# Optimization experiments

Hardware: AMD Instinct MI355X
Metric: run time of the kernel (lower is better)

The kernel has to match this reference:

```python
import jax, jax.numpy as jnp
import numpy as np

B, T, D = 8, 2048, 128


def setup_inputs() -> dict:
    key = jax.random.key(0)
    kq, kk, kv = jax.random.split(key, 3)
    q = jax.random.normal(kq, (B, T, D), dtype=jnp.float32)
    k = jax.random.normal(kk, (B, T, D), dtype=jnp.float32)
    v = jax.random.normal(kv, (B, T, D), dtype=jnp.float32)
    # causal mask, broadcast over batch; 0 -> masked
    mask = jnp.tril(jnp.ones((T, T), dtype=jnp.int32))[None, :, :]
    mode = jnp.float32(0.5)  # learnable scalar parameter (init 0.5)
    return {"q": q, "k": k, "v": v, "mask": mask, "mode": mode}


def reference(q, k, v, mask, mode):
    scale = D ** (-0.5)
    # meson score: -(Q K^T) * scale
    meson = -jnp.einsum("btd,bsd->bts", q, k) * scale
    # baryon score: Q against K with feature dim rolled by 1
    k_perm = jnp.roll(k, shift=1, axis=-1)
    baryon = jnp.einsum("btd,bsd->bts", q, k_perm) * scale
    alpha = jax.nn.sigmoid(mode)
    attn = alpha * meson + (1.0 - alpha) * baryon
    attn = jnp.where(mask == 0, -jnp.inf, attn)
    attn = jax.nn.softmax(attn, axis=-1)
    return jnp.einsum("bts,bsd->btd", attn, v)
```

## Files before the change

kernel.cpp:

```cpp
#include <hip/hip_runtime.h>
#include <hip/hip_bf16.h>
#include <cstdint>
#include <cstddef>


typedef __attribute__((ext_vector_type(8))) short short8;
typedef __attribute__((ext_vector_type(4))) float f32x4;

#define T_DIM 2048
#define D_DIM 128
#define B_DIM 8
#define SEGT 8
#define POSLOTS_PER_B 112
#define MLSLOTS_PER_B 144
#define LOG2E 1.4426950408889634f

__device__ __forceinline__ unsigned short f2bf(float f) {
  unsigned u = __builtin_bit_cast(unsigned, f);
  u += 0x7FFFu + ((u >> 16) & 1u);
  return (unsigned short)(u >> 16);
}
__device__ __forceinline__ float bf2f(unsigned short u) {
  return __uint_as_float(((unsigned)u) << 16);
}
__device__ __forceinline__ void gload_lds16(const void* g, void* l) {
  __builtin_amdgcn_global_load_lds(
      (const __attribute__((address_space(1))) unsigned int*)g,
      (__attribute__((address_space(3))) unsigned int*)l, 16, 0, 0);
}

__global__ __launch_bounds__(256) void prep_all(
    const float* __restrict__ q, const float* __restrict__ k, const float* __restrict__ v,
    const float* __restrict__ modep,
    unsigned short* __restrict__ qbf, unsigned short* __restrict__ kbf,
    unsigned short* __restrict__ vt)
{
  __shared__ unsigned short tile[64 * 136];
  const int b = blockIdx.x, s0 = blockIdx.y * 64;
  const int tid = threadIdx.x;
  const float alpha = 1.f / (1.f + __expf(-modep[0]));
  const float scale = 0.08838834764831845f;
  const float ca = -alpha * scale * LOG2E, cb = (1.f - alpha) * scale * LOG2E;

#pragma unroll
  for (int u = 0; u < 4; ++u) {
    int c = u * 256 + tid;
    int r = c >> 4, c8 = c & 15;
    size_t row = (size_t)b * T_DIM + s0 + r;
    float4 ka = *(const float4*)(k + row * D_DIM + c8 * 8);
    float4 kb2 = *(const float4*)(k + row * D_DIM + c8 * 8 + 4);
    short8 ko = { (short)f2bf(ka.x), (short)f2bf(ka.y), (short)f2bf(ka.z), (short)f2bf(ka.w),
                  (short)f2bf(kb2.x), (short)f2bf(kb2.y), (short)f2bf(kb2.z), (short)f2bf(kb2.w) };
    *(short8*)(kbf + row * D_DIM + c8 * 8) = ko;
    const float* qr = q + row * D_DIM;
    float e[9];
    float4 f0 = *(const float4*)(qr + c8 * 8);
    float4 f1 = *(const float4*)(qr + c8 * 8 + 4);
    e[0] = f0.x; e[1] = f0.y; e[2] = f0.z; e[3] = f0.w;
    e[4] = f1.x; e[5] = f1.y; e[6] = f1.z; e[7] = f1.w;
    e[8] = qr[(c8 * 8 + 8) & 127];
    short8 qo;
#pragma unroll
    for (int j = 0; j < 8; ++j) qo[j] = (short)f2bf(ca * e[j] + cb * e[j + 1]);
    *(short8*)(qbf + row * D_DIM + c8 * 8) = qo;
    float4 va = *(const float4*)(v + row * D_DIM + c8 * 8);
    float4 vb2 = *(const float4*)(v + row * D_DIM + c8 * 8 + 4);
    short8 vo = { (short)f2bf(va.x), (short)f2bf(va.y), (short)f2bf(va.z), (short)f2bf(va.w),
                  (short)f2bf(vb2.x), (short)f2bf(vb2.y), (short)f2bf(vb2.z), (short)f2bf(vb2.w) };
    *(short8*)(tile + r * 136 + c8 * 8) = vo;
  }
  __syncthreads();
#pragma unroll
  for (int u = 0; u < 8; ++u) {
    int c = u * 256 + tid;
    int d = c >> 4, sq = c & 15;
    ushort4 o = { tile[(sq * 4 + 0) * 136 + d], tile[(sq * 4 + 1) * 136 + d],
                  tile[(sq * 4 + 2) * 136 + d], tile[(sq * 4 + 3) * 136 + d] };
    *(ushort4*)(vt + ((size_t)b * D_DIM + d) * T_DIM + s0 + sq * 4) = o;
  }
}

__global__ __launch_bounds__(128, 2) void attn_kernel(
    const unsigned short* __restrict__ qbf, const unsigned short* __restrict__ kbf,
    const unsigned short* __restrict__ vt, float* __restrict__ out,
    unsigned short* __restrict__ po, float* __restrict__ ml)
{
  __shared__ uint4 smem4[2304];
  char* smem = (char*)smem4;
  const int tid = threadIdx.x;
  const int w = tid >> 6, lane = tid & 63;
  const int t16 = lane & 15, g = lane >> 4;
  const int b = blockIdx.x;
  const int c = 31 - (int)blockIdx.y;
  const int s = blockIdx.z;
  const int nt = 2 * c + 2;
  const int nseg = (c + 4) >> 2;
  if (s >= nseg) return;
  const int t0 = s * SEGT;
  const int t1 = min(nt, t0 + SEGT);
  const int qbw = c * 64 + w * 32;

  char* pw = smem + 32768 + w * 2048;
  const unsigned short* kbase = kbf + (size_t)b * T_DIM * D_DIM;
  const unsigned short* vbase = vt + (size_t)b * D_DIM * T_DIM;

  short8 qf[2][4];
#pragma unroll
  for (int mt = 0; mt < 2; ++mt) {
    const unsigned short* qr = qbf + ((size_t)b * T_DIM + qbw + mt * 16 + t16) * D_DIM + g * 8;
#pragma unroll
    for (int dd = 0; dd < 4; ++dd) qf[mt][dd] = *(const short8*)(qr + dd * 32);
  }

  f32x4 acc[2][8];
#pragma unroll
  for (int mt = 0; mt < 2; ++mt)
#pragma unroll
    for (int dt = 0; dt < 8; ++dt) acc[mt][dt] = (f32x4){0.f, 0.f, 0.f, 0.f};
  float mrun[2][4], lsum[2][4];
#pragma unroll
  for (int mt = 0; mt < 2; ++mt)
#pragma unroll
    for (int r = 0; r < 4; ++r) { mrun[mt][r] = -1e30f; lsum[mt][r] = 0.f; }

  auto stage = [&](int cur, int kt) {
    const int kv0 = kt * 32;
    char* kb = smem + cur * 8192;
    char* vb = smem + 16384 + cur * 8192;
#pragma unroll
    for (int u = 0; u < 4; ++u) {
      int s_loc = w * 16 + u * 4 + (lane >> 4);
      int slot = (lane & 15) ^ (s_loc & 7);
      gload_lds16(kbase + (size_t)(kv0 + s_loc) * D_DIM + slot * 8,
                  kb + w * 4096 + u * 1024);
    }
#pragma unroll
    for (int u = 0; u < 4; ++u) {
      int d_loc = w * 64 + u * 16 + (lane >> 2);
      int vslot = (lane & 3) ^ (d_loc & 3);
      gload_lds16(vbase + (size_t)d_loc * T_DIM + kv0 + vslot * 8,
                  vb + w * 4096 + u * 1024);
    }
  };

  stage(0, t0);
  __syncthreads();
  int cur = 0;

  for (int kt = t0; kt < t1; ++kt) {
    if (kt + 1 < t1) stage(cur ^ 1, kt + 1);
    const int kv0 = kt * 32;

    if (kv0 <= qbw + 31) {
      char* kb = smem + cur * 8192;
      char* vb = smem + 16384 + cur * 8192;

      f32x4 sj[2][2];
#pragma unroll
      for (int jt = 0; jt < 2; ++jt) {
        int srow = jt * 16 + t16;
        int rb = srow * 256, swz = (srow & 7) << 4;
        f32x4 s0 = (f32x4){0.f, 0.f, 0.f, 0.f};
        f32x4 s1 = (f32x4){0.f, 0.f, 0.f, 0.f};
#pragma unroll
        for (int dd = 0; dd < 4; ++dd) {
          short8 kf = *(const short8*)(kb + ((rb + dd * 64 + g * 16) ^ swz));
          s0 = __builtin_amdgcn_mfma_f32_16x16x32_bf16(qf[0][dd], kf, s0, 0, 0, 0);
          s1 = __builtin_amdgcn_mfma_f32_16x16x32_bf16(qf[1][dd], kf, s1, 0, 0, 0);
        }
        sj[0][jt] = s0; sj[1][jt] = s1;
      }

      if (kv0 == qbw) {
#pragma unroll
        for (int mt = 0; mt < 2; ++mt)
#pragma unroll
          for (int jt = 0; jt < 2; ++jt) {
            int sg = kv0 + jt * 16 + t16;
#pragma unroll
            for (int r = 0; r < 4; ++r) {
              int tg = qbw + mt * 16 + 4 * g + r;
              if (sg > tg) sj[mt][jt][r] = -1e30f;
            }
          }
      }

      float lm[2][4];
      int ok = 1;
#pragma unroll
      for (int mt = 0; mt < 2; ++mt)
#pragma unroll
        for (int r = 0; r < 4; ++r) {
          lm[mt][r] = fmaxf(sj[mt][0][r], sj[mt][1][r]);
          ok &= (lm[mt][r] <= mrun[mt][r] + 11.0f);
        }
      if (!__all(ok)) {
#pragma unroll
        for (int mt = 0; mt < 2; ++mt)
#pragma unroll
          for (int r = 0; r < 4; ++r) {
            float tm = lm[mt][r];
            tm = fmaxf(tm, __shfl_xor(tm, 1));
            tm = fmaxf(tm, __shfl_xor(tm, 2));
            tm = fmaxf(tm, __shfl_xor(tm, 4));
            tm = fmaxf(tm, __shfl_xor(tm, 8));
            float mnew = fmaxf(mrun[mt][r], tm);
            float corr = exp2f(mrun[mt][r] - mnew);
            mrun[mt][r] = mnew;
            lsum[mt][r] *= corr;
#pragma unroll
            for (int dt = 0; dt < 8; ++dt) acc[mt][dt][r] *= corr;
          }
      }

#pragma unroll
      for (int mt = 0; mt < 2; ++mt)
#pragma unroll
        for (int jt = 0; jt < 2; ++jt)
#pragma unroll
          for (int r = 0; r < 4; ++r) {
            float p = exp2f(sj[mt][jt][r] - mrun[mt][r]);
            lsum[mt][r] += p;
            int row = 4 * g + r;
            *(unsigned short*)(pw + mt * 1024 + row * 64 +
                               ((jt * 32 + t16 * 2) ^ ((row >> 2) << 4))) = f2bf(p);
          }

      short8 pf0 = *(const short8*)(pw + t16 * 64 + ((g * 16) ^ ((t16 >> 2) << 4)));
      short8 pf1 = *(const short8*)(pw + 1024 + t16 * 64 + ((g * 16) ^ ((t16 >> 2) << 4)));
#pragma unroll
      for (int dt = 0; dt < 8; ++dt) {
        int d = dt * 16 + t16;
        short8 vf = *(const short8*)(vb + d * 64 + ((g * 16) ^ ((d & 3) << 4)));
        acc[0][dt] = __builtin_amdgcn_mfma_f32_16x16x32_bf16(pf0, vf, acc[0][dt], 0, 0, 0);
        acc[1][dt] = __builtin_amdgcn_mfma_f32_16x16x32_bf16(pf1, vf, acc[1][dt], 0, 0, 0);
      }
    }

    __syncthreads();
    cur ^= 1;
  }

  float lred[2][4];
#pragma unroll
  for (int mt = 0; mt < 2; ++mt)
#pragma unroll
    for (int r = 0; r < 4; ++r) {
      float v0 = lsum[mt][r];
      v0 += __shfl_xor(v0, 1);
      v0 += __shfl_xor(v0, 2);
      v0 += __shfl_xor(v0, 4);
      v0 += __shfl_xor(v0, 8);
      lred[mt][r] = v0;
    }

  if (nseg == 1) {
#pragma unroll
    for (int mt = 0; mt < 2; ++mt)
#pragma unroll
      for (int r = 0; r < 4; ++r) {
        float inv = 1.0f / lred[mt][r];
#pragma unroll
        for (int dt = 0; dt < 8; ++dt)
          out[((size_t)b * T_DIM + qbw + mt * 16 + 4 * g + r) * D_DIM + dt * 16 + t16] =
              acc[mt][dt][r] * inv;
      }
  } else {
    int pofs = 0;
    for (int cc = 0; cc < c; ++cc) pofs += ((cc + 4) >> 2) - 1;
    if (s == 0) {
#pragma unroll
      for (int mt = 0; mt < 2; ++mt)
#pragma unroll
        for (int r = 0; r < 4; ++r)
#pragma unroll
          for (int dt = 0; dt < 8; ++dt)
            out[((size_t)b * T_DIM + qbw + mt * 16 + 4 * g + r) * D_DIM + dt * 16 + t16] =
                acc[mt][dt][r];
    } else {
      unsigned short* pob = po + ((size_t)b * POSLOTS_PER_B + pofs + (s - 1)) * 8192;
#pragma unroll
      for (int mt = 0; mt < 2; ++mt)
#pragma unroll
        for (int r = 0; r < 4; ++r) {
          int rb = w * 32 + mt * 16 + 4 * g + r;
#pragma unroll
          for (int dt = 0; dt < 8; ++dt)
            pob[rb * 128 + dt * 16 + t16] = f2bf(acc[mt][dt][r]);
        }
    }
    if (t16 == 0) {
      const size_t mlslot = (size_t)b * MLSLOTS_PER_B + pofs + c + s;
#pragma unroll
      for (int mt = 0; mt < 2; ++mt)
#pragma unroll
        for (int r = 0; r < 4; ++r) {
          int rb = w * 32 + mt * 16 + 4 * g + r;
          ml[mlslot * 128 + rb] = mrun[mt][r];
          ml[mlslot * 128 + 64 + rb] = lred[mt][r];
        }
    }
  }
}

__global__ __launch_bounds__(256) void combine_kernel(
    const unsigned short* __restrict__ po, const float* __restrict__ ml,
    float* __restrict__ out)
{
  const int tid = threadIdx.x;
  const int b = blockIdx.x;
  const int c = 4 + (int)blockIdx.y;
  const int nseg = (c + 4) >> 2;
  int pofs = 0;
  for (int cc = 0; cc < c; ++cc) pofs += ((cc + 4) >> 2) - 1;
  const size_t mlbase = (size_t)b * MLSLOTS_PER_B + pofs + c;
  const size_t pobase = (size_t)b * POSLOTS_PER_B + pofs;

  __shared__ float wgt[64][8];
  if (tid < 64) {
    float M = -1e30f;
    for (int s = 0; s < nseg; ++s)
      M = fmaxf(M, ml[(mlbase + s) * 128 + tid]);
    float L = 0.f;
    for (int s = 0; s < nseg; ++s) {
      float e = exp2f(ml[(mlbase + s) * 128 + tid] - M);
      wgt[tid][s] = e;
      L += e * ml[(mlbase + s) * 128 + 64 + tid];
    }
    float invL = 1.f / L;
    for (int s = 0; s < nseg; ++s) wgt[tid][s] *= invL;
  }
  __syncthreads();

#pragma unroll
  for (int it = 0; it < 4; ++it) {
    int vid = it * 256 + tid;
    int r = vid >> 4, ch = vid & 15;
    float* op = out + ((size_t)b * T_DIM + c * 64 + r) * D_DIM + ch * 8;
    float4 a0 = *(const float4*)op;
    float4 a1 = *(const float4*)(op + 4);
    float w0 = wgt[r][0];
    float o[8] = { w0 * a0.x, w0 * a0.y, w0 * a0.z, w0 * a0.w,
                   w0 * a1.x, w0 * a1.y, w0 * a1.z, w0 * a1.w };
    for (int s = 1; s < nseg; ++s) {
      short8 pv = *(const short8*)(po + (pobase + s - 1) * 8192 + r * 128 + ch * 8);
      float ws = wgt[r][s];
#pragma unroll
      for (int j = 0; j < 8; ++j) o[j] += ws * bf2f((unsigned short)pv[j]);
    }
    *(float4*)op = (float4){o[0], o[1], o[2], o[3]};
    *(float4*)(op + 4) = (float4){o[4], o[5], o[6], o[7]};
  }
}

extern "C" void kernel_launch(void* const* d_in, const int* in_sizes, int n_in,
                              void* d_out, int out_size, void* d_ws, size_t ws_size,
                              hipStream_t stream) {
  const float* q = (const float*)d_in[0];
  const float* k = (const float*)d_in[1];
  const float* v = (const float*)d_in[2];
  const float* mode = (const float*)d_in[4];
  float* out = (float*)d_out;

  char* ws = (char*)d_ws;
  unsigned short* qbf = (unsigned short*)(ws);
  unsigned short* kbf = (unsigned short*)(ws + 4194304);
  unsigned short* vtb = (unsigned short*)(ws + 8388608);
  unsigned short* po  = (unsigned short*)(ws + 12582912);
  float*          ml  = (float*)(ws + 27262976);

  prep_all<<<dim3(B_DIM, T_DIM / 64), 256, 0, stream>>>(q, k, v, mode, qbf, kbf, vtb);
  attn_kernel<<<dim3(B_DIM, 32, SEGT), 128, 0, stream>>>(qbf, kbf, vtb, out, po, ml);
  combine_kernel<<<dim3(B_DIM, 28), 256, 0, stream>>>(po, ml, out);
}
```

Baseline: 56.85 us.

## Switch attention to 32x32x16 MFMA with transposed S and register-shuffled P

Rewrites the attention inner loop to use 32x32x16 bf16 MFMAs that compute S transposed (K as A operand), so each lane owns one query row. The softmax row max and sum then need only a single cross-half shuffle, and P is repacked into the B-operand layout with lane shuffles instead of a round trip through LDS. This removes the per-wave P scratch buffer and the LDS swizzle writes and reads, and widens the K swizzle to 16 slots. Output stores become vectorized per row. The cost is larger accumulator fragments per lane and possible register pressure under the 2-block launch bound.

```diff
diff --git a/kernel.cpp b/kernel.cpp
--- a/kernel.cpp
+++ b/kernel.cpp
@@ -6,6 +6,8 @@
 
 typedef __attribute__((ext_vector_type(8))) short short8;
 typedef __attribute__((ext_vector_type(4))) float f32x4;
+typedef __attribute__((ext_vector_type(16))) float f32x16;
+typedef __attribute__((ext_vector_type(4))) unsigned uint4v;
 
 #define T_DIM 2048
 #define D_DIM 128
@@ -22,6 +24,9 @@
 }
 __device__ __forceinline__ float bf2f(unsigned short u) {
   return __uint_as_float(((unsigned)u) << 16);
+}
+__device__ __forceinline__ unsigned pack2bf(float a, float b) {
+  return (unsigned)f2bf(a) | ((unsigned)f2bf(b) << 16);
 }
 __device__ __forceinline__ void gload_lds16(const void* g, void* l) {
   __builtin_amdgcn_global_load_lds(
@@ -85,11 +90,11 @@
     const unsigned short* __restrict__ vt, float* __restrict__ out,
     unsigned short* __restrict__ po, float* __restrict__ ml)
 {
-  __shared__ uint4 smem4[2304];
+  __shared__ uint4 smem4[2048];
   char* smem = (char*)smem4;
   const int tid = threadIdx.x;
   const int w = tid >> 6, lane = tid & 63;
-  const int t16 = lane & 15, g = lane >> 4;
+  const int q32 = lane & 31, h = lane >> 5;
   const int b = blockIdx.x;
   const int c = 31 - (int)blockIdx.y;
   const int s = blockIdx.z;
@@ -99,29 +104,22 @@
   const int t0 = s * SEGT;
   const int t1 = min(nt, t0 + SEGT);
   const int qbw = c * 64 + w * 32;
-
-  char* pw = smem + 32768 + w * 2048;
+  const int qg = qbw + q32;
+
   const unsigned short* kbase = kbf + (size_t)b * T_DIM * D_DIM;
   const unsigned short* vbase = vt + (size_t)b * D_DIM * T_DIM;
 
-  short8 qf[2][4];
-#pragma unroll
-  for (int mt = 0; mt < 2; ++mt) {
-    const unsigned short* qr = qbf + ((size_t)b * T_DIM + qbw + mt * 16 + t16) * D_DIM + g * 8;
-#pragma unroll
-    for (int dd = 0; dd < 4; ++dd) qf[mt][dd] = *(const short8*)(qr + dd * 32);
-  }
-
-  f32x4 acc[2][8];
-#pragma unroll
-  for (int mt = 0; mt < 2; ++mt)
-#pragma unroll
-    for (int dt = 0; dt < 8; ++dt) acc[mt][dt] = (f32x4){0.f, 0.f, 0.f, 0.f};
-  float mrun[2][4], lsum[2][4];
-#pragma unroll
-  for (int mt = 0; mt < 2; ++mt)
-#pragma unroll
-    for (int r = 0; r < 4; ++r) { mrun[mt][r] = -1e30f; lsum[mt][r] = 0.f; }
+  short8 qf[8];
+  {
+    const unsigned short* qr = qbf + ((size_t)b * T_DIM + qg) * D_DIM;
+#pragma unroll
+    for (int j = 0; j < 8; ++j) qf[j] = *(const short8*)(qr + (2 * j + h) * 8);
+  }
+
+  f32x16 acc[4];
+#pragma unroll
+  for (int dt = 0; dt < 4; ++dt) acc[dt] = (f32x16)(0.f);
+  float mrun = -1e30f, lsum = 0.f;
 
   auto stage = [&](int cur, int kt) {
     const int kv0 = kt * 32;
@@ -130,7 +128,7 @@
 #pragma unroll
     for (int u = 0; u < 4; ++u) {
       int s_loc = w * 16 + u * 4 + (lane >> 4);
-      int slot = (lane & 15) ^ (s_loc & 7);
+      int slot = (lane & 15) ^ (s_loc & 15);
       gload_lds16(kbase + (size_t)(kv0 + s_loc) * D_DIM + slot * 8,
                   kb + w * 4096 + u * 1024);
     }
@@ -155,85 +153,69 @@
       char* kb = smem + cur * 8192;
       char* vb = smem + 16384 + cur * 8192;
 
-      f32x4 sj[2][2];
-#pragma unroll
-      for (int jt = 0; jt < 2; ++jt) {
-        int srow = jt * 16 + t16;
-        int rb = srow * 256, swz = (srow & 7) << 4;
-        f32x4 s0 = (f32x4){0.f, 0.f, 0.f, 0.f};
-        f32x4 s1 = (f32x4){0.f, 0.f, 0.f, 0.f};
-#pragma unroll
-        for (int dd = 0; dd < 4; ++dd) {
-          short8 kf = *(const short8*)(kb + ((rb + dd * 64 + g * 16) ^ swz));
-          s0 = __builtin_amdgcn_mfma_f32_16x16x32_bf16(qf[0][dd], kf, s0, 0, 0, 0);
-          s1 = __builtin_amdgcn_mfma_f32_16x16x32_bf16(qf[1][dd], kf, s1, 0, 0, 0);
+      f32x16 sj = (f32x16)(0.f);
+#pragma unroll
+      for (int j = 0; j < 8; ++j) {
+        int r = q32;
+        short8 kf = *(const short8*)(kb + r * 256 + (((2 * j + h) ^ (r & 15)) << 4));
+        sj = __builtin_amdgcn_mfma_f32_32x32x16_bf16(kf, qf[j], sj, 0, 0, 0);
+      }
+
+      if (kv0 == qbw) {
+#pragma unroll
+        for (int r = 0; r < 16; ++r) {
+          int kvg = kv0 + (r & 3) + 8 * (r >> 2) + 4 * h;
+          if (kvg > qg) sj[r] = -1e30f;
         }
-        sj[0][jt] = s0; sj[1][jt] = s1;
-      }
-
-      if (kv0 == qbw) {
-#pragma unroll
-        for (int mt = 0; mt < 2; ++mt)
-#pragma unroll
-          for (int jt = 0; jt < 2; ++jt) {
-            int sg = kv0 + jt * 16 + t16;
-#pragma unroll
-            for (int r = 0; r < 4; ++r) {
-              int tg = qbw + mt * 16 + 4 * g + r;
-              if (sg > tg) sj[mt][jt][r] = -1e30f;
-            }
-          }
-      }
-
-      float lm[2][4];
-      int ok = 1;
-#pragma unroll
-      for (int mt = 0; mt < 2; ++mt)
-#pragma unroll
-        for (int r = 0; r < 4; ++r) {
-          lm[mt][r] = fmaxf(sj[mt][0][r], sj[mt][1][r]);
-          ok &= (lm[mt][r] <= mrun[mt][r] + 11.0f);
+      }
+
+      float lm = sj[0];
+#pragma unroll
+      for (int r = 1; r < 16; ++r) lm = fmaxf(lm, sj[r]);
+      int ok = (lm <= mrun + 11.0f);
+      if (!__all(ok)) {
+        float tm = fmaxf(lm, __shfl_xor(lm, 32));
+        float mnew = fmaxf(mrun, tm);
+        float corr = exp2f(mrun - mnew);
+        mrun = mnew;
+        lsum *= corr;
+#pragma unroll
+        for (int dt = 0; dt < 4; ++dt) acc[dt] *= corr;
+      }
+
+      float ls = 0.f;
+#pragma unroll
+      for (int r = 0; r < 16; ++r) {
+        float p = exp2f(sj[r] - mrun);
+        sj[r] = p;
+        ls += p;
+      }
+      lsum += ls;
+
+      unsigned W[8];
+#pragma unroll
+      for (int t = 0; t < 8; ++t) W[t] = pack2bf(sj[2 * t], sj[2 * t + 1]);
+      short8 pf[2];
+#pragma unroll
+      for (int j = 0; j < 2; ++j) {
+        unsigned w0 = W[4 * j + 0], w1 = W[4 * j + 1];
+        unsigned w2 = W[4 * j + 2], w3 = W[4 * j + 3];
+        unsigned s0 = (unsigned)__shfl_xor((int)w0, 32);
+        unsigned s1 = (unsigned)__shfl_xor((int)w1, 32);
+        unsigned s2 = (unsigned)__shfl_xor((int)w2, 32);
+        unsigned s3 = (unsigned)__shfl_xor((int)w3, 32);
+        uint4v bw = { h ? s2 : w0, h ? s3 : w1, h ? w2 : s0, h ? w3 : s1 };
+        pf[j] = __builtin_bit_cast(short8, bw);
+      }
+
+#pragma unroll
+      for (int dt = 0; dt < 4; ++dt) {
+        int d = dt * 32 + q32;
+#pragma unroll
+        for (int j = 0; j < 2; ++j) {
+          short8 vf = *(const short8*)(vb + d * 64 + (((2 * j + h) ^ (d & 3)) << 4));
+          acc[dt] = __builtin_amdgcn_mfma_f32_32x32x16_bf16(vf, pf[j], acc[dt], 0, 0, 0);
         }
-      if (!__all(ok)) {
-#pragma unroll
-        for (int mt = 0; mt < 2; ++mt)
-#pragma unroll
-          for (int r = 0; r < 4; ++r) {
-            float tm = lm[mt][r];
-            tm = fmaxf(tm, __shfl_xor(tm, 1));
-            tm = fmaxf(tm, __shfl_xor(tm, 2));
-            tm = fmaxf(tm, __shfl_xor(tm, 4));
-            tm = fmaxf(tm, __shfl_xor(tm, 8));
-            float mnew = fmaxf(mrun[mt][r], tm);
-            float corr = exp2f(mrun[mt][r] - mnew);
-            mrun[mt][r] = mnew;
-            lsum[mt][r] *= corr;
-#pragma unroll
-            for (int dt = 0; dt < 8; ++dt) acc[mt][dt][r] *= corr;
-          }
-      }
-
-#pragma unroll
-      for (int mt = 0; mt < 2; ++mt)
-#pragma unroll
-        for (int jt = 0; jt < 2; ++jt)
-#pragma unroll
-          for (int r = 0; r < 4; ++r) {
-            float p = exp2f(sj[mt][jt][r] - mrun[mt][r]);
-            lsum[mt][r] += p;
-            int row = 4 * g + r;
-            *(unsigned short*)(pw + mt * 1024 + row * 64 +
-                               ((jt * 32 + t16 * 2) ^ ((row >> 2) << 4))) = f2bf(p);
-          }
-
-      short8 pf0 = *(const short8*)(pw + t16 * 64 + ((g * 16) ^ ((t16 >> 2) << 4)));
-      short8 pf1 = *(const short8*)(pw + 1024 + t16 * 64 + ((g * 16) ^ ((t16 >> 2) << 4)));
-#pragma unroll
-      for (int dt = 0; dt < 8; ++dt) {
-        int d = dt * 16 + t16;
-        short8 vf = *(const short8*)(vb + d * 64 + ((g * 16) ^ ((d & 3) << 4)));
-        acc[0][dt] = __builtin_amdgcn_mfma_f32_16x16x32_bf16(pf0, vf, acc[0][dt], 0, 0, 0);
-        acc[1][dt] = __builtin_amdgcn_mfma_f32_16x16x32_bf16(pf1, vf, acc[1][dt], 0, 0, 0);
       }
     }
 
@@ -241,64 +223,52 @@
     cur ^= 1;
   }
 
-  float lred[2][4];
-#pragma unroll
-  for (int mt = 0; mt < 2; ++mt)
-#pragma unroll
-    for (int r = 0; r < 4; ++r) {
-      float v0 = lsum[mt][r];
-      v0 += __shfl_xor(v0, 1);
-      v0 += __shfl_xor(v0, 2);
-      v0 += __shfl_xor(v0, 4);
-      v0 += __shfl_xor(v0, 8);
-      lred[mt][r] = v0;
-    }
+  float lred = lsum + __shfl_xor(lsum, 32);
 
   if (nseg == 1) {
-#pragma unroll
-    for (int mt = 0; mt < 2; ++mt)
-#pragma unroll
-      for (int r = 0; r < 4; ++r) {
-        float inv = 1.0f / lred[mt][r];
-#pragma unroll
-        for (int dt = 0; dt < 8; ++dt)
-          out[((size_t)b * T_DIM + qbw + mt * 16 + 4 * g + r) * D_DIM + dt * 16 + t16] =
-              acc[mt][dt][r] * inv;
+    float inv = 1.0f / lred;
+    float* orow = out + ((size_t)b * T_DIM + qg) * D_DIM;
+#pragma unroll
+    for (int dt = 0; dt < 4; ++dt)
+#pragma unroll
+      for (int rg = 0; rg < 4; ++rg) {
+        int d0 = dt * 32 + rg * 8 + 4 * h;
+        f32x4 o = { acc[dt][4 * rg] * inv, acc[dt][4 * rg + 1] * inv,
+                    acc[dt][4 * rg + 2] * inv, acc[dt][4 * rg + 3] * inv };
+        *(f32x4*)(orow + d0) = o;
       }
   } else {
     int pofs = 0;
     for (int cc = 0; cc < c; ++cc) pofs += ((cc + 4) >> 2) - 1;
     if (s == 0) {
-#pragma unroll
-      for (int mt = 0; mt < 2; ++mt)
-#pragma unroll
-        for (int r = 0; r < 4; ++r)
-#pragma unroll
-          for (int dt = 0; dt < 8; ++dt)
-            out[((size_t)b * T_DIM + qbw + mt * 16 + 4 * g + r) * D_DIM + dt * 16 + t16] =
-                acc[mt][dt][r];
+      float* orow = out + ((size_t)b * T_DIM + qg) * D_DIM;
+#pragma unroll
+      for (int dt = 0; dt < 4; ++dt)
+#pragma unroll
+        for (int rg = 0; rg < 4; ++rg) {
+          int d0 = dt * 32 + rg * 8 + 4 * h;
+          f32x4 o = { acc[dt][4 * rg], acc[dt][4 * rg + 1],
+                      acc[dt][4 * rg + 2], acc[dt][4 * rg + 3] };
+          *(f32x4*)(orow + d0) = o;
+        }
     } else {
-      unsigned short* pob = po + ((size_t)b * POSLOTS_PER_B + pofs + (s - 1)) * 8192;
-#pragma unroll
-      for (int mt = 0; mt < 2; ++mt)
-#pragma unroll
-        for (int r = 0; r < 4; ++r) {
-          int rb = w * 32 + mt * 16 + 4 * g + r;
-#pragma unroll
-          for (int dt = 0; dt < 8; ++dt)
-            pob[rb * 128 + dt * 16 + t16] = f2bf(acc[mt][dt][r]);
+      unsigned short* prow = po + ((size_t)b * POSLOTS_PER_B + pofs + (s - 1)) * 8192 +
+                             (w * 32 + q32) * 128;
+#pragma unroll
+      for (int dt = 0; dt < 4; ++dt)
+#pragma unroll
+        for (int rg = 0; rg < 4; ++rg) {
+          int d0 = dt * 32 + rg * 8 + 4 * h;
+          ushort4 o = { f2bf(acc[dt][4 * rg]), f2bf(acc[dt][4 * rg + 1]),
+                        f2bf(acc[dt][4 * rg + 2]), f2bf(acc[dt][4 * rg + 3]) };
+          *(ushort4*)(prow + d0) = o;
         }
     }
-    if (t16 == 0) {
+    if (h == 0) {
       const size_t mlslot = (size_t)b * MLSLOTS_PER_B + pofs + c + s;
-#pragma unroll
-      for (int mt = 0; mt < 2; ++mt)
-#pragma unroll
-        for (int r = 0; r < 4; ++r) {
-          int rb = w * 32 + mt * 16 + 4 * g + r;
-          ml[mlslot * 128 + rb] = mrun[mt][r];
-          ml[mlslot * 128 + 64 + rb] = lred[mt][r];
-        }
+      int rb = w * 32 + q32;
+      ml[mlslot * 128 + rb] = mrun;
+      ml[mlslot * 128 + 64 + rb] = lred;
     }
   }
 }
```

Result: no change. 57.23 us (+0.7%).
